# Kernel optimization log

Measured on AMD Instinct MI355X. Metric: run time of the kernel, lower is better.

Reference implementation:

```python
import jax, jax.numpy as jnp
import numpy as np

N_X, N_U, N_Y = 256, 32, 32
BATCH, T = 16, 8192
LAM_MIN, LAM_MAX = 0.9, 0.995
B_SCALE, D_SCALE = 0.25, 0.25


def setup_inputs() -> dict:
    key = jax.random.key(0)
    k = jax.random.split(key, 6)
    # Orthogonal Q via QR of a random Gaussian matrix (as in the torch module)
    M = jax.random.normal(k[0], (N_X, N_X), dtype=jnp.float32)
    Q, _ = jnp.linalg.qr(M)
    lam = LAM_MIN + (LAM_MAX - LAM_MIN) * jax.random.uniform(k[1], (N_X,), dtype=jnp.float32)
    Bmat = B_SCALE * jax.random.normal(k[2], (N_X, N_U), dtype=jnp.float32)
    # C picks out the first n_y coordinates (C[i, i] = 1)
    C = jnp.eye(N_Y, N_X, dtype=jnp.float32)
    D = D_SCALE * jax.random.normal(k[3], (N_Y, N_U), dtype=jnp.float32)
    x0 = jax.random.normal(k[4], (BATCH, N_X), dtype=jnp.float32)
    u = jax.random.normal(k[5], (BATCH, T, N_U), dtype=jnp.float32)
    return {"x0": x0, "u": u, "Q": Q, "lam": lam, "Bmat": Bmat, "C": C, "D": D}


def _diag_scan(lam, v):
    """Diagonal linear recurrence x_t = lam * x_{t-1} + v_t (x_0 folded into v[:, 0]).

    lam: (N,), v: (B, T, N) -> states x_1..x_T of shape (B, T, N).
    """
    a = jnp.broadcast_to(lam, v.shape)

    def op(l, r):
        a1, b1 = l
        a2, b2 = r
        return a1 * a2, a2 * b1 + b2

    return jax.lax.associative_scan(op, (a, v), axis=1)[1]


def reference(x0, u, Q, lam, Bmat, C, D):
    Bz = Q.T @ Bmat            # (n_x, n_u) modal input matrix
    Cz = C @ Q                 # (n_y, n_x) modal output matrix
    z0 = x0 @ Q                # (B, n_x)   modal initial state
    v = jnp.einsum('btu,nu->btn', u, Bz)   # (B, T, n_x)
    v = v.at[:, 0].add(lam * z0)            # fold lam * z0 into first step
    z_next = _diag_scan(lam, v)             # (B, T, n_x) = z_1..z_T
    # y_t uses z_t for t = 0..T-1 (states[:, :-1] in the original)
    z_prev = jnp.concatenate([z0[:, None, :], z_next[:, :-1]], axis=1)
    y = jnp.einsum('btn,yn->bty', z_prev, Cz) + jnp.einsum('btu,yu->bty', u, D)
    return y
```

## Files before the change

kernel.cpp:

```cpp
#include <hip/hip_runtime.h>

typedef _Float16 half4_t __attribute__((ext_vector_type(4)));
typedef _Float16 half8_t __attribute__((ext_vector_type(8)));
typedef float f32x4 __attribute__((ext_vector_type(4)));

constexpr int NX = 256, NU = 32, NY = 32, BATCH = 16, T = 8192;
constexpr int NC = 64, L = 128;
constexpr int SUBT = 32, NSUB = L / SUBT;
constexpr int ZP = 264;

__device__ __forceinline__ half8_t cvt8(float4 a, float4 b) {
    half8_t h;
    h[0] = (_Float16)a.x; h[1] = (_Float16)a.y; h[2] = (_Float16)a.z; h[3] = (_Float16)a.w;
    h[4] = (_Float16)b.x; h[5] = (_Float16)b.y; h[6] = (_Float16)b.z; h[7] = (_Float16)b.w;
    return h;
}

__global__ __launch_bounds__(256) void k_pre(
    const float* __restrict__ x0, const float* __restrict__ Q,
    const float* __restrict__ Bm,
    _Float16* __restrict__ Bzh, float* __restrict__ z0)
{
    int o = blockIdx.x * 64 + (threadIdx.x >> 2);
    int p = threadIdx.x & 3;
    if (o >= 12288) return;
    float s = 0.f;
    int k0 = p * 64;
    if (o < 8192) {
        int n = o >> 5, j = o & 31;
        for (int k = k0; k < k0 + 64; ++k) s = fmaf(Q[k * NX + n], Bm[k * NU + j], s);
    } else {
        int g = o - 8192; int b = g >> 8, nn = g & 255;
        for (int k = k0; k < k0 + 64; ++k) s = fmaf(x0[b * NX + k], Q[k * NX + nn], s);
    }
    s += __shfl_xor(s, 1);
    s += __shfl_xor(s, 2);
    if (p == 0) {
        if (o < 8192) Bzh[o] = (_Float16)s;
        else          z0[o - 8192] = s;
    }
}

__global__ __launch_bounds__(256) void k_phase1(
    const float* __restrict__ u, const float* __restrict__ lam,
    const _Float16* __restrict__ Bzh, float* __restrict__ S)
{
    const int b = blockIdx.x >> 6, c = blockIdx.x & 63, tid = threadIdx.x;
    const int w = tid >> 6, lane = tid & 63, m16 = lane & 15, quad = lane >> 4;

    const float* ug = u + ((size_t)(b * T) + (size_t)c * L) * NU;
    const float* r0 = ug + (size_t)m16 * NU + quad * 8;
    const float* r1 = ug + (size_t)(16 + m16) * NU + quad * 8;

    float4 c0a = *(const float4*)r0, c0b = *(const float4*)(r0 + 4);
    float4 c1a = *(const float4*)r1, c1b = *(const float4*)(r1 + 4);

    half8_t bfrag[4];
    #pragma unroll
    for (int i = 0; i < 4; ++i)
        bfrag[i] = *(const half8_t*)&Bzh[((4 * w + i) * 16 + m16) * NU + quad * 8];

    float wr[4][4], wt16[4], l32[4], acc[4];
    #pragma unroll
    for (int i = 0; i < 4; ++i) {
        float la = lam[(4 * w + i) * 16 + m16];
        float p2 = la * la, p4 = p2 * p2, p8 = p4 * p4, p16 = p8 * p8;
        float inv1 = 1.0f / la;
        float inv4 = (inv1 * inv1) * (inv1 * inv1);
        float pq = 1.0f;
        if (quad & 1) pq *= inv4;
        if (quad & 2) pq *= inv4 * inv4;
        float w0 = (p16 * p8 * p4 * p2 * la) * pq;
        wr[i][0] = w0;
        wr[i][1] = w0 * inv1;
        wr[i][2] = wr[i][1] * inv1;
        wr[i][3] = wr[i][2] * inv1;
        wt16[i] = 1.0f / p16;
        l32[i] = p16 * p16;
        acc[i] = 0.f;
    }

    for (int sub = 0; sub < NSUB; ++sub) {
        half8_t af0 = cvt8(c0a, c0b);
        half8_t af1 = cvt8(c1a, c1b);
        if (sub < NSUB - 1) {
            const float* n0 = r0 + (size_t)(sub + 1) * SUBT * NU;
            const float* n1 = r1 + (size_t)(sub + 1) * SUBT * NU;
            c0a = *(const float4*)n0; c0b = *(const float4*)(n0 + 4);
            c1a = *(const float4*)n1; c1b = *(const float4*)(n1 + 4);
        }
        #pragma unroll
        for (int i = 0; i < 4; ++i) {
            f32x4 z4 = {0.f, 0.f, 0.f, 0.f};
            f32x4 v0 = __builtin_amdgcn_mfma_f32_16x16x32_f16(af0, bfrag[i], z4, 0, 0, 0);
            f32x4 v1 = __builtin_amdgcn_mfma_f32_16x16x32_f16(af1, bfrag[i], z4, 0, 0, 0);
            float s0 = wr[i][0] * v0[0] + wr[i][1] * v0[1] + wr[i][2] * v0[2] + wr[i][3] * v0[3];
            float s1 = wr[i][0] * v1[0] + wr[i][1] * v1[1] + wr[i][2] * v1[2] + wr[i][3] * v1[3];
            acc[i] = fmaf(l32[i], acc[i], fmaf(wt16[i], s1, s0));
        }
    }
    #pragma unroll
    for (int i = 0; i < 4; ++i) {
        acc[i] += __shfl_xor(acc[i], 16);
        acc[i] += __shfl_xor(acc[i], 32);
    }
    float out = quad == 0 ? acc[0] : quad == 1 ? acc[1] : quad == 2 ? acc[2] : acc[3];
    S[(size_t)blockIdx.x * NX + (4 * w + quad) * 16 + m16] = out;
}

__global__ __launch_bounds__(256) void k_phase3(
    const float* __restrict__ u, const float* __restrict__ lam,
    const _Float16* __restrict__ Bzh, const float* __restrict__ Q,
    const float* __restrict__ D, const float* __restrict__ S,
    const float* __restrict__ z0, float* __restrict__ y)
{
    __shared__ __align__(16) _Float16 zt[SUBT][ZP];
    __shared__ float pvec[NX];

    const int b = blockIdx.x >> 6, c = blockIdx.x & 63, tid = threadIdx.x;
    const int w = tid >> 6, lane = tid & 63, m16 = lane & 15, quad = lane >> 4;
    const int tw = w & 1, yw = w >> 1;

    const float* ug = u + ((size_t)(b * T) + (size_t)c * L) * NU;
    const float* r0 = ug + (size_t)m16 * NU + quad * 8;
    const float* r1 = ug + (size_t)(16 + m16) * NU + quad * 8;

    float4 c0a = *(const float4*)r0, c0b = *(const float4*)(r0 + 4);
    float4 c1a = *(const float4*)r1, c1b = *(const float4*)(r1 + 4);

    {
        float la = lam[tid];
        float l2L = 128.0f * __log2f(la);
        const float* Sb = S + (size_t)(b * NC) * NX + tid;
        float pv = 0.f;
        #pragma unroll 8
        for (int k = 0; k < c; ++k) {
            float wgt = exp2f((float)k * l2L);
            pv = fmaf(wgt, Sb[(size_t)(c - 1 - k) * NX], pv);
        }
        pvec[tid] = fmaf(exp2f((float)c * l2L), z0[b * NX + tid], pv);
    }

    half8_t bfrag[4];
    #pragma unroll
    for (int i = 0; i < 4; ++i)
        bfrag[i] = *(const half8_t*)&Bzh[((4 * w + i) * 16 + m16) * NU + quad * 8];
    half8_t wfrag[9];
    #pragma unroll
    for (int kk = 0; kk < 8; ++kk) {
        float4 qa = *(const float4*)&Q[(size_t)(yw * 16 + m16) * NX + kk * 32 + quad * 8];
        float4 qb = *(const float4*)&Q[(size_t)(yw * 16 + m16) * NX + kk * 32 + quad * 8 + 4];
        wfrag[kk] = cvt8(qa, qb);
    }
    {
        float4 da = *(const float4*)&D[(size_t)(yw * 16 + m16) * NU + quad * 8];
        float4 db = *(const float4*)&D[(size_t)(yw * 16 + m16) * NU + quad * 8 + 4];
        wfrag[8] = cvt8(da, db);
    }

    float lamn[4], inv1[4], iq[4], i16p[4], fq[4], f16p[4], l32[4], p[4];
    #pragma unroll
    for (int i = 0; i < 4; ++i) {
        int ni = (4 * w + i) * 16 + m16;
        float la = lam[ni];
        lamn[i] = la;
        float p2 = la * la, p4 = p2 * p2, p8 = p4 * p4, p16 = p8 * p8;
        float iv = 1.0f / la;
        inv1[i] = iv;
        float iv4 = (iv * iv) * (iv * iv);
        float pqi = 1.0f, pqf = 1.0f;
        if (quad & 1) { pqi *= iv4; pqf *= p4; }
        if (quad & 2) { pqi *= iv4 * iv4; pqf *= p8; }
        iq[i] = iv * pqi;
        fq[i] = pqf;
        i16p[i] = 1.0f / p16;
        f16p[i] = p16;
        l32[i] = p16 * p16;
    }
    __syncthreads();
    #pragma unroll
    for (int i = 0; i < 4; ++i)
        p[i] = pvec[(4 * w + i) * 16 + m16];

    float* yg = y + ((size_t)(b * T) + (size_t)c * L) * NY;

    for (int sub = 0; sub < NSUB; ++sub) {
        half8_t af0 = cvt8(c0a, c0b);
        half8_t af1 = cvt8(c1a, c1b);
        if (sub < NSUB - 1) {
            const float* n0 = r0 + (size_t)(sub + 1) * SUBT * NU;
            const float* n1 = r1 + (size_t)(sub + 1) * SUBT * NU;
            c0a = *(const float4*)n0; c0b = *(const float4*)(n0 + 4);
            c1a = *(const float4*)n1; c1b = *(const float4*)(n1 + 4);
        }
        #pragma unroll
        for (int i = 0; i < 4; ++i) {
            int ni = (4 * w + i) * 16 + m16;
            f32x4 z4 = {0.f, 0.f, 0.f, 0.f};
            f32x4 v0 = __builtin_amdgcn_mfma_f32_16x16x32_f16(af0, bfrag[i], z4, 0, 0, 0);
            f32x4 v1 = __builtin_amdgcn_mfma_f32_16x16x32_f16(af1, bfrag[i], z4, 0, 0, 0);
            float a0[4], a1[4];
            float sc = iq[i];
            #pragma unroll
            for (int r = 0; r < 4; ++r) {
                a0[r] = v0[r] * sc;
                a1[r] = v1[r] * (sc * i16p[i]);
                sc *= inv1[i];
            }
            float e0[4], e1[4];
            e0[0] = 0.f; e0[1] = a0[0]; e0[2] = e0[1] + a0[1]; e0[3] = e0[2] + a0[2];
            float S40 = e0[3] + a0[3];
            e1[0] = 0.f; e1[1] = a1[0]; e1[2] = e1[1] + a1[1]; e1[3] = e1[2] + a1[2];
            float S41 = e1[3] + a1[3];
            float incl0 = S40;
            float t0 = __shfl_up(incl0, 16); if (quad >= 1) incl0 += t0;
            t0 = __shfl_up(incl0, 32);       if (quad >= 2) incl0 += t0;
            float excl0 = incl0 - S40;
            float total0 = __shfl(incl0, 48 + m16);
            float incl1 = S41;
            float t1 = __shfl_up(incl1, 16); if (quad >= 1) incl1 += t1;
            t1 = __shfl_up(incl1, 32);       if (quad >= 2) incl1 += t1;
            float excl1 = incl1 - S41;
            float total1 = __shfl(incl1, 48 + m16);
            float f = fq[i];
            #pragma unroll
            for (int r = 0; r < 4; ++r) {
                float zv0 = f * (p[i] + (excl0 + e0[r]));
                float zv1 = (f * f16p[i]) * (p[i] + (total0 + excl1 + e1[r]));
                zt[quad * 4 + r][ni] = (_Float16)zv0;
                zt[16 + quad * 4 + r][ni] = (_Float16)zv1;
                f *= lamn[i];
            }
            p[i] = l32[i] * (p[i] + (total0 + total1));
        }
        __syncthreads();

        f32x4 acc = {0.f, 0.f, 0.f, 0.f};
        #pragma unroll
        for (int kk = 0; kk < 8; ++kk) {
            half8_t az = *(const half8_t*)&zt[tw * 16 + m16][kk * 32 + quad * 8];
            acc = __builtin_amdgcn_mfma_f32_16x16x32_f16(wfrag[kk], az, acc, 0, 0, 0);
        }
        {
            half8_t au = tw ? af1 : af0;
            acc = __builtin_amdgcn_mfma_f32_16x16x32_f16(wfrag[8], au, acc, 0, 0, 0);
        }
        {
            float4 v = make_float4(acc[0], acc[1], acc[2], acc[3]);
            *(float4*)&yg[(size_t)(sub * SUBT + tw * 16 + m16) * NY + yw * 16 + quad * 4] = v;
        }
        if (sub < NSUB - 1)
            __syncthreads();
    }
}

extern "C" void kernel_launch(void* const* d_in, const int* in_sizes, int n_in,
                              void* d_out, int out_size, void* d_ws, size_t ws_size,
                              hipStream_t stream) {
    (void)in_sizes; (void)n_in; (void)out_size; (void)ws_size;
    const float* x0  = (const float*)d_in[0];
    const float* u   = (const float*)d_in[1];
    const float* Q   = (const float*)d_in[2];
    const float* lam = (const float*)d_in[3];
    const float* Bm  = (const float*)d_in[4];
    const float* D   = (const float*)d_in[6];
    float* y = (float*)d_out;

    char* ws = (char*)d_ws;
    _Float16* Bzh = (_Float16*)(ws);
    float*    z0  = (float*)(ws + 16384);
    float*    S   = (float*)(ws + 32768);

    k_pre   <<<192, 256, 0, stream>>>(x0, Q, Bm, Bzh, z0);
    k_phase1<<<BATCH * NC, 256, 0, stream>>>(u, lam, Bzh, S);
    k_phase3<<<BATCH * NC, 256, 0, stream>>>(u, lam, Bzh, Q, D, S, z0, y);
}
```

Measured before the change: 129.7 us.

## Stage u through swizzled LDS and process two chunks per phase3 block

Both phase kernels now load u with coalesced float4 loads by thread id, convert it to fp16 into a swizzled shared-memory tile, and read the MFMA fragments back from LDS. The per-row strided global fragment loads are gone. Phase3 now handles two adjacent chunks per block: it halves the grid, computes the second chunk's prefix state from the first with one extra step, and double-buffers the u tiles with prefetch two sub-blocks ahead. This cuts the redundant prefix-state loops and raises the work per sync, at the cost of more LDS and registers and fewer blocks (512) to spread across the CUs.

```diff
diff --git a/kernel.cpp b/kernel.cpp
--- a/kernel.cpp
+++ b/kernel.cpp
@@ -45,15 +45,10 @@
     const float* __restrict__ u, const float* __restrict__ lam,
     const _Float16* __restrict__ Bzh, float* __restrict__ S)
 {
+    __shared__ __align__(16) _Float16 ut[2][SUBT][32];
+
     const int b = blockIdx.x >> 6, c = blockIdx.x & 63, tid = threadIdx.x;
     const int w = tid >> 6, lane = tid & 63, m16 = lane & 15, quad = lane >> 4;
-
-    const float* ug = u + ((size_t)(b * T) + (size_t)c * L) * NU;
-    const float* r0 = ug + (size_t)m16 * NU + quad * 8;
-    const float* r1 = ug + (size_t)(16 + m16) * NU + quad * 8;
-
-    float4 c0a = *(const float4*)r0, c0b = *(const float4*)(r0 + 4);
-    float4 c1a = *(const float4*)r1, c1b = *(const float4*)(r1 + 4);
 
     half8_t bfrag[4];
     #pragma unroll
@@ -80,15 +75,20 @@
         acc[i] = 0.f;
     }
 
+    const float* ug = u + ((size_t)(b * T) + (size_t)c * L) * NU;
+
     for (int sub = 0; sub < NSUB; ++sub) {
-        half8_t af0 = cvt8(c0a, c0b);
-        half8_t af1 = cvt8(c1a, c1b);
-        if (sub < NSUB - 1) {
-            const float* n0 = r0 + (size_t)(sub + 1) * SUBT * NU;
-            const float* n1 = r1 + (size_t)(sub + 1) * SUBT * NU;
-            c0a = *(const float4*)n0; c0b = *(const float4*)(n0 + 4);
-            c1a = *(const float4*)n1; c1b = *(const float4*)(n1 + 4);
-        }
+        {
+            float4 uu = *(const float4*)(ug + (size_t)sub * SUBT * NU + tid * 4);
+            int tr = tid >> 3, cb = ((tid & 7) * 4 + (tr & 3) * 8) & 31;
+            half4_t h; h.x = (_Float16)uu.x; h.y = (_Float16)uu.y;
+            h.z = (_Float16)uu.z; h.w = (_Float16)uu.w;
+            *(half4_t*)&ut[sub & 1][tr][cb] = h;
+        }
+        __syncthreads();
+        int rot = (m16 & 3) * 8;
+        half8_t af0 = *(const half8_t*)&ut[sub & 1][m16][(quad * 8 + rot) & 31];
+        half8_t af1 = *(const half8_t*)&ut[sub & 1][16 + m16][(quad * 8 + rot) & 31];
         #pragma unroll
         for (int i = 0; i < 4; ++i) {
             f32x4 z4 = {0.f, 0.f, 0.f, 0.f};
@@ -114,19 +114,21 @@
     const float* __restrict__ D, const float* __restrict__ S,
     const float* __restrict__ z0, float* __restrict__ y)
 {
-    __shared__ __align__(16) _Float16 zt[SUBT][ZP];
-    __shared__ float pvec[NX];
-
-    const int b = blockIdx.x >> 6, c = blockIdx.x & 63, tid = threadIdx.x;
+    __shared__ __align__(16) _Float16 ut[2][2][SUBT][32];
+    __shared__ __align__(16) _Float16 zt[2][SUBT][ZP];
+    __shared__ float pvec[2][NX];
+
+    const int bx = blockIdx.x, b = bx >> 5, ci = bx & 31, tid = threadIdx.x;
+    const int cA = 2 * ci, cB = 2 * ci + 1;
     const int w = tid >> 6, lane = tid & 63, m16 = lane & 15, quad = lane >> 4;
     const int tw = w & 1, yw = w >> 1;
-
-    const float* ug = u + ((size_t)(b * T) + (size_t)c * L) * NU;
-    const float* r0 = ug + (size_t)m16 * NU + quad * 8;
-    const float* r1 = ug + (size_t)(16 + m16) * NU + quad * 8;
-
-    float4 c0a = *(const float4*)r0, c0b = *(const float4*)(r0 + 4);
-    float4 c1a = *(const float4*)r1, c1b = *(const float4*)(r1 + 4);
+    const int rot = (m16 & 3) * 8;
+    const int tr = tid >> 3, cb = ((tid & 7) * 4 + (tr & 3) * 8) & 31;
+
+    const float* ugA = u + ((size_t)(b * T) + (size_t)cA * L) * NU;
+    const float* ugB = u + ((size_t)(b * T) + (size_t)cB * L) * NU;
+    float4 ucA = *(const float4*)(ugA + tid * 4);
+    float4 ucB = *(const float4*)(ugB + tid * 4);
 
     {
         float la = lam[tid];
@@ -134,11 +136,13 @@
         const float* Sb = S + (size_t)(b * NC) * NX + tid;
         float pv = 0.f;
         #pragma unroll 8
-        for (int k = 0; k < c; ++k) {
+        for (int k = 0; k < cA; ++k) {
             float wgt = exp2f((float)k * l2L);
-            pv = fmaf(wgt, Sb[(size_t)(c - 1 - k) * NX], pv);
-        }
-        pvec[tid] = fmaf(exp2f((float)c * l2L), z0[b * NX + tid], pv);
+            pv = fmaf(wgt, Sb[(size_t)(cA - 1 - k) * NX], pv);
+        }
+        float pA = fmaf(exp2f((float)cA * l2L), z0[b * NX + tid], pv);
+        pvec[0][tid] = pA;
+        pvec[1][tid] = fmaf(exp2f(l2L), pA, Sb[(size_t)cA * NX]);
     }
 
     half8_t bfrag[4];
@@ -158,7 +162,7 @@
         wfrag[8] = cvt8(da, db);
     }
 
-    float lamn[4], inv1[4], iq[4], i16p[4], fq[4], f16p[4], l32[4], p[4];
+    float lamn[4], inv1[4], iq[4], i16p[4], fq[4], f16p[4], l32[4], pA[4], pB[4];
     #pragma unroll
     for (int i = 0; i < 4; ++i) {
         int ni = (4 * w + i) * 16 + m16;
@@ -177,75 +181,108 @@
         f16p[i] = p16;
         l32[i] = p16 * p16;
     }
+
+    {
+        half4_t hA; hA.x = (_Float16)ucA.x; hA.y = (_Float16)ucA.y;
+        hA.z = (_Float16)ucA.z; hA.w = (_Float16)ucA.w;
+        *(half4_t*)&ut[0][0][tr][cb] = hA;
+        half4_t hB; hB.x = (_Float16)ucB.x; hB.y = (_Float16)ucB.y;
+        hB.z = (_Float16)ucB.z; hB.w = (_Float16)ucB.w;
+        *(half4_t*)&ut[1][0][tr][cb] = hB;
+    }
     __syncthreads();
     #pragma unroll
-    for (int i = 0; i < 4; ++i)
-        p[i] = pvec[(4 * w + i) * 16 + m16];
-
-    float* yg = y + ((size_t)(b * T) + (size_t)c * L) * NY;
+    for (int i = 0; i < 4; ++i) {
+        pA[i] = pvec[0][(4 * w + i) * 16 + m16];
+        pB[i] = pvec[1][(4 * w + i) * 16 + m16];
+    }
+    float4 unA = *(const float4*)(ugA + (size_t)SUBT * NU + tid * 4);
+    float4 unB = *(const float4*)(ugB + (size_t)SUBT * NU + tid * 4);
+
+    float* ygA = y + ((size_t)(b * T) + (size_t)cA * L) * NY;
+    float* ygB = y + ((size_t)(b * T) + (size_t)cB * L) * NY;
+
+    half8_t afA0, afA1, afB0, afB1;
 
     for (int sub = 0; sub < NSUB; ++sub) {
-        half8_t af0 = cvt8(c0a, c0b);
-        half8_t af1 = cvt8(c1a, c1b);
+        afA0 = *(const half8_t*)&ut[0][sub & 1][m16][(quad * 8 + rot) & 31];
+        afA1 = *(const half8_t*)&ut[0][sub & 1][16 + m16][(quad * 8 + rot) & 31];
+        afB0 = *(const half8_t*)&ut[1][sub & 1][m16][(quad * 8 + rot) & 31];
+        afB1 = *(const half8_t*)&ut[1][sub & 1][16 + m16][(quad * 8 + rot) & 31];
+        if (sub < NSUB - 2) {
+            ucA = *(const float4*)(ugA + (size_t)(sub + 2) * SUBT * NU + tid * 4);
+            ucB = *(const float4*)(ugB + (size_t)(sub + 2) * SUBT * NU + tid * 4);
+        }
+        #pragma unroll
+        for (int st = 0; st < 2; ++st) {
+            half8_t af0 = st ? afB0 : afA0;
+            half8_t af1 = st ? afB1 : afA1;
+            float*  pp  = st ? pB : pA;
+            #pragma unroll
+            for (int i = 0; i < 4; ++i) {
+                int ni = (4 * w + i) * 16 + m16;
+                f32x4 z4 = {0.f, 0.f, 0.f, 0.f};
+                f32x4 v0 = __builtin_amdgcn_mfma_f32_16x16x32_f16(af0, bfrag[i], z4, 0, 0, 0);
+                f32x4 v1 = __builtin_amdgcn_mfma_f32_16x16x32_f16(af1, bfrag[i], z4, 0, 0, 0);
+                float a0[4], a1[4];
+                float sc = iq[i];
+                #pragma unroll
+                for (int r = 0; r < 4; ++r) {
+                    a0[r] = v0[r] * sc;
+                    a1[r] = v1[r] * (sc * i16p[i]);
+                    sc *= inv1[i];
+                }
+                float e0[4], e1[4];
+                e0[0] = 0.f; e0[1] = a0[0]; e0[2] = e0[1] + a0[1]; e0[3] = e0[2] + a0[2];
+                float S40 = e0[3] + a0[3];
+                e1[0] = 0.f; e1[1] = a1[0]; e1[2] = e1[1] + a1[1]; e1[3] = e1[2] + a1[2];
+                float S41 = e1[3] + a1[3];
+                float incl0 = S40;
+                float t0 = __shfl_up(incl0, 16); if (quad >= 1) incl0 += t0;
+                t0 = __shfl_up(incl0, 32);       if (quad >= 2) incl0 += t0;
+                float excl0 = incl0 - S40;
+                float total0 = __shfl(incl0, 48 + m16);
+                float incl1 = S41;
+                float t1 = __shfl_up(incl1, 16); if (quad >= 1) incl1 += t1;
+                t1 = __shfl_up(incl1, 32);       if (quad >= 2) incl1 += t1;
+                float excl1 = incl1 - S41;
+                float total1 = __shfl(incl1, 48 + m16);
+                float f = fq[i];
+                #pragma unroll
+                for (int r = 0; r < 4; ++r) {
+                    float zv0 = f * (pp[i] + (excl0 + e0[r]));
+                    float zv1 = (f * f16p[i]) * (pp[i] + (total0 + excl1 + e1[r]));
+                    zt[st][quad * 4 + r][ni] = (_Float16)zv0;
+                    zt[st][16 + quad * 4 + r][ni] = (_Float16)zv1;
+                    f *= lamn[i];
+                }
+                pp[i] = l32[i] * (pp[i] + (total0 + total1));
+            }
+        }
         if (sub < NSUB - 1) {
-            const float* n0 = r0 + (size_t)(sub + 1) * SUBT * NU;
-            const float* n1 = r1 + (size_t)(sub + 1) * SUBT * NU;
-            c0a = *(const float4*)n0; c0b = *(const float4*)(n0 + 4);
-            c1a = *(const float4*)n1; c1b = *(const float4*)(n1 + 4);
-        }
+            half4_t hA; hA.x = (_Float16)unA.x; hA.y = (_Float16)unA.y;
+            hA.z = (_Float16)unA.z; hA.w = (_Float16)unA.w;
+            *(half4_t*)&ut[0][(sub + 1) & 1][tr][cb] = hA;
+            half4_t hB; hB.x = (_Float16)unB.x; hB.y = (_Float16)unB.y;
+            hB.z = (_Float16)unB.z; hB.w = (_Float16)unB.w;
+            *(half4_t*)&ut[1][(sub + 1) & 1][tr][cb] = hB;
+            unA = ucA; unB = ucB;
+        }
+        __syncthreads();
+
         #pragma unroll
-        for (int i = 0; i < 4; ++i) {
-            int ni = (4 * w + i) * 16 + m16;
-            f32x4 z4 = {0.f, 0.f, 0.f, 0.f};
-            f32x4 v0 = __builtin_amdgcn_mfma_f32_16x16x32_f16(af0, bfrag[i], z4, 0, 0, 0);
-            f32x4 v1 = __builtin_amdgcn_mfma_f32_16x16x32_f16(af1, bfrag[i], z4, 0, 0, 0);
-            float a0[4], a1[4];
-            float sc = iq[i];
+        for (int st = 0; st < 2; ++st) {
+            f32x4 acc = {0.f, 0.f, 0.f, 0.f};
             #pragma unroll
-            for (int r = 0; r < 4; ++r) {
-                a0[r] = v0[r] * sc;
-                a1[r] = v1[r] * (sc * i16p[i]);
-                sc *= inv1[i];
+            for (int kk = 0; kk < 8; ++kk) {
+                half8_t az = *(const half8_t*)&zt[st][tw * 16 + m16][kk * 32 + quad * 8];
+                acc = __builtin_amdgcn_mfma_f32_16x16x32_f16(wfrag[kk], az, acc, 0, 0, 0);
             }
-            float e0[4], e1[4];
-            e0[0] = 0.f; e0[1] = a0[0]; e0[2] = e0[1] + a0[1]; e0[3] = e0[2] + a0[2];
-            float S40 = e0[3] + a0[3];
-            e1[0] = 0.f; e1[1] = a1[0]; e1[2] = e1[1] + a1[1]; e1[3] = e1[2] + a1[2];
-            float S41 = e1[3] + a1[3];
-            float incl0 = S40;
-            float t0 = __shfl_up(incl0, 16); if (quad >= 1) incl0 += t0;
-            t0 = __shfl_up(incl0, 32);       if (quad >= 2) incl0 += t0;
-            float excl0 = incl0 - S40;
-            float total0 = __shfl(incl0, 48 + m16);
-            float incl1 = S41;
-            float t1 = __shfl_up(incl1, 16); if (quad >= 1) incl1 += t1;
-            t1 = __shfl_up(incl1, 32);       if (quad >= 2) incl1 += t1;
-            float excl1 = incl1 - S41;
-            float total1 = __shfl(incl1, 48 + m16);
-            float f = fq[i];
-            #pragma unroll
-            for (int r = 0; r < 4; ++r) {
-                float zv0 = f * (p[i] + (excl0 + e0[r]));
-                float zv1 = (f * f16p[i]) * (p[i] + (total0 + excl1 + e1[r]));
-                zt[quad * 4 + r][ni] = (_Float16)zv0;
-                zt[16 + quad * 4 + r][ni] = (_Float16)zv1;
-                f *= lamn[i];
+            {
+                half8_t au = st ? (tw ? afB1 : afB0) : (tw ? afA1 : afA0);
+                acc = __builtin_amdgcn_mfma_f32_16x16x32_f16(wfrag[8], au, acc, 0, 0, 0);
             }
-            p[i] = l32[i] * (p[i] + (total0 + total1));
-        }
-        __syncthreads();
-
-        f32x4 acc = {0.f, 0.f, 0.f, 0.f};
-        #pragma unroll
-        for (int kk = 0; kk < 8; ++kk) {
-            half8_t az = *(const half8_t*)&zt[tw * 16 + m16][kk * 32 + quad * 8];
-            acc = __builtin_amdgcn_mfma_f32_16x16x32_f16(wfrag[kk], az, acc, 0, 0, 0);
-        }
-        {
-            half8_t au = tw ? af1 : af0;
-            acc = __builtin_amdgcn_mfma_f32_16x16x32_f16(wfrag[8], au, acc, 0, 0, 0);
-        }
-        {
+            float* yg = st ? ygB : ygA;
             float4 v = make_float4(acc[0], acc[1], acc[2], acc[3]);
             *(float4*)&yg[(size_t)(sub * SUBT + tw * 16 + m16) * NY + yw * 16 + quad * 4] = v;
         }
@@ -273,5 +310,5 @@
 
     k_pre   <<<192, 256, 0, stream>>>(x0, Q, Bm, Bzh, z0);
     k_phase1<<<BATCH * NC, 256, 0, stream>>>(u, lam, Bzh, S);
-    k_phase3<<<BATCH * NC, 256, 0, stream>>>(u, lam, Bzh, Q, D, S, z0, y);
-}
+    k_phase3<<<BATCH * NC / 2, 256, 0, stream>>>(u, lam, Bzh, Q, D, S, z0, y);
+}
```

New measurement: 114.3 us, median of 2. 1.13x faster.
